# Performance work log

Hardware: AMD Instinct MI355X
Metric: run time of the kernel (lower is better)

## Reference

```python
import jax, jax.numpy as jnp
import numpy as np

EMBED_DIM = 256
NUM_HEADS = 8
PROJ_DIM = EMBED_DIM // NUM_HEADS


def setup_inputs() -> dict:
    key = jax.random.key(0)
    ks = jax.random.split(key, 5)
    scale = 1.0 / np.sqrt(EMBED_DIM)
    inputs = jax.random.normal(ks[0], (2, 12, 12, 12, EMBED_DIM), dtype=jnp.float32)
    Wq = jax.random.normal(ks[1], (EMBED_DIM, EMBED_DIM), dtype=jnp.float32) * scale
    Wk = jax.random.normal(ks[2], (EMBED_DIM, EMBED_DIM), dtype=jnp.float32) * scale
    Wv = jax.random.normal(ks[3], (EMBED_DIM, EMBED_DIM), dtype=jnp.float32) * scale
    Wo = jax.random.normal(ks[4], (EMBED_DIM, EMBED_DIM), dtype=jnp.float32) * scale
    z = jnp.zeros((EMBED_DIM,), dtype=jnp.float32)
    return {"inputs": inputs, "Wq": Wq, "bq": z, "Wk": Wk, "bk": z,
            "Wv": Wv, "bv": z, "Wo": Wo, "bo": z}


def reference(inputs, Wq, bq, Wk, bk, Wv, bv, Wo, bo):
    B, h, w, d, E = inputs.shape
    S = h * w * d  # flattened spatial sequence
    x = inputs.reshape(B, S, E)
    # projections + head split: [B, S, E] -> [B, H, S, P]
    def split_heads(t):
        return t.reshape(B, S, NUM_HEADS, PROJ_DIM).transpose(0, 2, 1, 3)
    q = split_heads(x @ Wq + bq)
    k = split_heads(x @ Wk + bk)
    v = split_heads(x @ Wv + bv)
    # NOTE: original module does NOT scale by 1/sqrt(proj_dim)
    scores = jnp.einsum('bhsp,bhtp->bhst', q, k)  # [B, H, S, S]
    attn = jax.nn.softmax(scores, axis=-1)
    out = jnp.einsum('bhst,bhtp->bhsp', attn, v)  # [B, H, S, P]
    out = out.transpose(0, 2, 1, 3).reshape(B, h, w, d, E)
    return out @ Wo + bo
```

## Files before the change

kernel.cpp:

```cpp
#include <hip/hip_runtime.h>
#include <math.h>

#define EMBED 256
#define HEADS 8
#define PDIM  32
#define BATCH 2
#define SEQ   1728
#define NTOK  (BATCH*SEQ)
#define NE    (NTOK*EMBED)
#define NKT   (SEQ/64)
#define LOG2E 1.44269504088896f

typedef __attribute__((ext_vector_type(8))) __bf16 bf16x8;
typedef __attribute__((ext_vector_type(4))) float  f32x4;
typedef unsigned short ushort_t;
typedef unsigned int   uint_t;

static __device__ __forceinline__ unsigned short f2bf_rne(float f) {
    union { float f; unsigned u; } x; x.f = f;
    unsigned r = x.u + 0x7fffu + ((x.u >> 16) & 1u);
    return (unsigned short)(r >> 16);
}
union v8cast { uint4 u; bf16x8 v; };

static __device__ __forceinline__ void cvt8_hilo(const float f[8], bf16x8& hi, bf16x8& lo) {
    uint4 ph, pl;
    uint_t* phv = (uint_t*)&ph; uint_t* plv = (uint_t*)&pl;
    #pragma unroll
    for (int j = 0; j < 4; ++j) {
        const float f0 = f[2 * j], f1 = f[2 * j + 1];
        const uint_t u0 = __float_as_uint(f0) + 0x8000u;
        const uint_t u1 = __float_as_uint(f1) + 0x8000u;
        phv[j] = __builtin_amdgcn_perm(u1, u0, 0x07060302u);
        const float l0 = f0 - __uint_as_float(u0 & 0xFFFF0000u);
        const float l1 = f1 - __uint_as_float(u1 & 0xFFFF0000u);
        plv[j] = __builtin_amdgcn_perm(__float_as_uint(l1) + 0x8000u,
                                       __float_as_uint(l0) + 0x8000u, 0x07060302u);
    }
    v8cast ch; ch.u = ph; hi = ch.v;
    v8cast cl; cl.u = pl; lo = cl.v;
}

__global__ __launch_bounds__(64) void qkv_gemm_kernel(
    const float* __restrict__ x,
    const float* __restrict__ Wq, const float* __restrict__ bq,
    const float* __restrict__ Wk, const float* __restrict__ bk,
    const float* __restrict__ Wv, const float* __restrict__ bv,
    ushort_t* __restrict__ qo, ushort_t* __restrict__ ko, ushort_t* __restrict__ vt)
{
    const int lane = threadIdx.x, li = lane & 15, quad = lane >> 4;
    const int m0 = blockIdx.x * 64, n0 = blockIdx.y * 32, z = blockIdx.z;
    const float* __restrict__ W    = (z == 0) ? Wq : (z == 1) ? Wk : Wv;
    const float* __restrict__ bias = (z == 0) ? bq : (z == 1) ? bk : bv;

    const float* ap = x + (size_t)(m0 + li) * EMBED + quad * 8;

    f32x4 acc[4][2];
    #pragma unroll
    for (int mt = 0; mt < 4; ++mt)
        #pragma unroll
        for (int nt = 0; nt < 2; ++nt)
            acc[mt][nt] = (f32x4){0.f, 0.f, 0.f, 0.f};

    #pragma unroll 2
    for (int k0 = 0; k0 < EMBED; k0 += 32) {
        bf16x8 ah[4], al[4];
        #pragma unroll
        for (int mt = 0; mt < 4; ++mt) {
            float af[8];
            *(float4*)&af[0] = *(const float4*)(ap + (size_t)mt * 16 * EMBED + k0);
            *(float4*)&af[4] = *(const float4*)(ap + (size_t)mt * 16 * EMBED + k0 + 4);
            cvt8_hilo(af, ah[mt], al[mt]);
        }
        bf16x8 bh[2], bl[2];
        #pragma unroll
        for (int nt = 0; nt < 2; ++nt) {
            const int n = n0 + nt * 16 + li;
            const float* wp = W + (size_t)(k0 + quad * 8) * EMBED + n;
            float bf[8];
            #pragma unroll
            for (int jj = 0; jj < 8; ++jj) bf[jj] = wp[(size_t)jj * EMBED];
            cvt8_hilo(bf, bh[nt], bl[nt]);
        }
        #pragma unroll
        for (int mt = 0; mt < 4; ++mt)
            #pragma unroll
            for (int nt = 0; nt < 2; ++nt) {
                acc[mt][nt] = __builtin_amdgcn_mfma_f32_16x16x32_bf16(ah[mt], bh[nt], acc[mt][nt], 0, 0, 0);
                acc[mt][nt] = __builtin_amdgcn_mfma_f32_16x16x32_bf16(al[mt], bh[nt], acc[mt][nt], 0, 0, 0);
                acc[mt][nt] = __builtin_amdgcn_mfma_f32_16x16x32_bf16(ah[mt], bl[nt], acc[mt][nt], 0, 0, 0);
            }
    }

    const int b = m0 / SEQ;
    const int sbase = m0 - b * SEQ;

    if (z <= 1) {
        ushort_t* __restrict__ dst = z ? ko : qo;
        #pragma unroll
        for (int nt = 0; nt < 2; ++nt) {
            const int gcol = n0 + nt * 16 + li;
            const int h = gcol >> 5, p = gcol & 31;
            const float bb = bias[gcol];
            ushort_t* base = dst + ((size_t)(b * HEADS + h) * SEQ) * PDIM + p;
            #pragma unroll
            for (int mt = 0; mt < 4; ++mt)
                #pragma unroll
                for (int r = 0; r < 4; ++r) {
                    const int s = sbase + mt * 16 + quad * 4 + r;
                    base[(size_t)s * PDIM] = f2bf_rne(acc[mt][nt][r] + bb);
                }
        }
    } else {
        #pragma unroll
        for (int nt = 0; nt < 2; ++nt) {
            const int gcol = n0 + nt * 16 + li;
            const int h = gcol >> 5, p = gcol & 31;
            const float bb = bias[gcol];
            ushort_t* base = vt + ((size_t)(b * HEADS + h) * PDIM + p) * SEQ;
            #pragma unroll
            for (int mt = 0; mt < 4; ++mt) {
                const int s0 = sbase + mt * 16 + quad * 4;
                ushort4 w;
                w.x = f2bf_rne(acc[mt][nt][0] + bb);
                w.y = f2bf_rne(acc[mt][nt][1] + bb);
                w.z = f2bf_rne(acc[mt][nt][2] + bb);
                w.w = f2bf_rne(acc[mt][nt][3] + bb);
                *(ushort4*)&base[s0] = w;
            }
        }
    }
}

__global__ __launch_bounds__(256) void attn_kernel(
    const ushort_t* __restrict__ q, const ushort_t* __restrict__ k,
    const ushort_t* __restrict__ vt, ushort_t* __restrict__ aob)
{
    const int t    = threadIdx.x;
    const int lane = t & 63;
    const int w    = t >> 6;
    const int li   = lane & 15;
    const int quad = lane >> 4;
    const int bh = blockIdx.y;
    const int b  = bh >> 3, h = bh & 7;
    const int q0 = blockIdx.x * 64 + w * 16;

    const ushort_t* __restrict__ qb = q  + (size_t)bh * SEQ * PDIM;
    const ushort_t* __restrict__ kb = k  + (size_t)bh * SEQ * PDIM;
    const ushort_t* __restrict__ vb = vt + (size_t)bh * PDIM * SEQ;

    __shared__ ushort_t Ks[2][64][40];
    __shared__ ushort_t Vs[2][32][72];
    __shared__ ushort_t Ps[4][16][72];

    const bf16x8 qfrag = *(const bf16x8*)(qb + (size_t)(q0 + li) * PDIM + quad * 8);

    const int jk = w * 16 + (lane >> 2), ck = (lane & 3) * 8;
    const int pv = w * 8 + (lane >> 3),  cv = (lane & 7) * 8;
    const ushort_t* kgp = kb + (size_t)jk * PDIM + ck;
    const ushort_t* vgp = vb + (size_t)pv * SEQ + cv;

    f32x4 o0 = {0.f, 0.f, 0.f, 0.f};
    f32x4 o1 = {0.f, 0.f, 0.f, 0.f};
    float m_run = -__builtin_inff(), l_run = 0.f;

    uint4 kreg = *(const uint4*)(kgp);
    uint4 vreg = *(const uint4*)(vgp);

    for (int kt = 0; kt < NKT; ++kt) {
        const int p = kt & 1;
        *(uint4*)&Ks[p][jk][ck] = kreg;
        *(uint4*)&Vs[p][pv][cv] = vreg;
        __syncthreads();
        if (kt + 1 < NKT) {
            kreg = *(const uint4*)(kgp + (size_t)(kt + 1) * 64 * PDIM);
            vreg = *(const uint4*)(vgp + (kt + 1) * 64);
        }

        const f32x4 zero = {0.f, 0.f, 0.f, 0.f};
        f32x4 st[4];
        #pragma unroll
        for (int jt = 0; jt < 4; ++jt) {
            const bf16x8 kf = *(const bf16x8*)&Ks[p][jt * 16 + li][quad * 8];
            st[jt] = __builtin_amdgcn_mfma_f32_16x16x32_bf16(kf, qfrag, zero, 0, 0, 0);
        }

        float tm = st[0][0];
        #pragma unroll
        for (int jt = 0; jt < 4; ++jt)
            #pragma unroll
            for (int r = 0; r < 4; ++r) tm = fmaxf(tm, st[jt][r]);
        tm = fmaxf(tm, __shfl_xor(tm, 16));
        tm = fmaxf(tm, __shfl_xor(tm, 32));
        const float mnew  = fmaxf(m_run, tm);
        const float negml = -(mnew * LOG2E);

        float ps = 0.f;
        #pragma unroll
        for (int jt = 0; jt < 4; ++jt) {
            const float p0 = __builtin_amdgcn_exp2f(fmaf(st[jt][0], LOG2E, negml));
            const float p1 = __builtin_amdgcn_exp2f(fmaf(st[jt][1], LOG2E, negml));
            const float p2 = __builtin_amdgcn_exp2f(fmaf(st[jt][2], LOG2E, negml));
            const float p3 = __builtin_amdgcn_exp2f(fmaf(st[jt][3], LOG2E, negml));
            ps += (p0 + p1) + (p2 + p3);
            uint2 pw;
            pw.x = __builtin_amdgcn_perm(__float_as_uint(p1) + 0x8000u,
                                         __float_as_uint(p0) + 0x8000u, 0x07060302u);
            pw.y = __builtin_amdgcn_perm(__float_as_uint(p3) + 0x8000u,
                                         __float_as_uint(p2) + 0x8000u, 0x07060302u);
            *(uint2*)&Ps[w][li][16 * jt + 4 * quad] = pw;
        }
        ps += __shfl_xor(ps, 16);
        ps += __shfl_xor(ps, 32);

        const float alpha = __builtin_amdgcn_exp2f(fmaf(m_run, LOG2E, negml));
        l_run = fmaf(l_run, alpha, ps);
        m_run = mnew;

        float af[4];
        #pragma unroll
        for (int r = 0; r < 4; ++r) af[r] = __shfl(alpha, 4 * quad + r);
        #pragma unroll
        for (int r = 0; r < 4; ++r) { o0[r] *= af[r]; o1[r] *= af[r]; }

        const bf16x8 pa0 = *(const bf16x8*)&Ps[w][li][8 * quad];
        const bf16x8 pa1 = *(const bf16x8*)&Ps[w][li][32 + 8 * quad];
        const bf16x8 vf00 = *(const bf16x8*)&Vs[p][li][quad * 8];
        const bf16x8 vf01 = *(const bf16x8*)&Vs[p][16 + li][quad * 8];
        const bf16x8 vf10 = *(const bf16x8*)&Vs[p][li][32 + quad * 8];
        const bf16x8 vf11 = *(const bf16x8*)&Vs[p][16 + li][32 + quad * 8];
        o0 = __builtin_amdgcn_mfma_f32_16x16x32_bf16(pa0, vf00, o0, 0, 0, 0);
        o0 = __builtin_amdgcn_mfma_f32_16x16x32_bf16(pa1, vf10, o0, 0, 0, 0);
        o1 = __builtin_amdgcn_mfma_f32_16x16x32_bf16(pa0, vf01, o1, 0, 0, 0);
        o1 = __builtin_amdgcn_mfma_f32_16x16x32_bf16(pa1, vf11, o1, 0, 0, 0);
    }

    float linv[4];
    #pragma unroll
    for (int r = 0; r < 4; ++r) linv[r] = 1.0f / __shfl(l_run, 4 * quad + r);
    #pragma unroll
    for (int r = 0; r < 4; ++r) {
        const int s = q0 + 4 * quad + r;
        ushort_t* row = aob + ((size_t)(b * SEQ + s)) * EMBED + h * PDIM;
        row[li]      = f2bf_rne(o0[r] * linv[r]);
        row[16 + li] = f2bf_rne(o1[r] * linv[r]);
    }
}

__global__ __launch_bounds__(64) void out_gemm_kernel(
    const ushort_t* __restrict__ a, const float* __restrict__ Wo,
    const float* __restrict__ bo, float* __restrict__ out)
{
    const int lane = threadIdx.x, li = lane & 15, quad = lane >> 4;
    const int m0 = blockIdx.x * 64, n0 = blockIdx.y * 16;

    const ushort_t* aph = a + (size_t)(m0 + li) * EMBED + quad * 8;

    f32x4 acc[4];
    #pragma unroll
    for (int mt = 0; mt < 4; ++mt) acc[mt] = (f32x4){0.f, 0.f, 0.f, 0.f};

    #pragma unroll 2
    for (int k0 = 0; k0 < EMBED; k0 += 32) {
        bf16x8 ah[4];
        #pragma unroll
        for (int mt = 0; mt < 4; ++mt)
            ah[mt] = *(const bf16x8*)(aph + (size_t)mt * 16 * EMBED + k0);
        const float* wp = Wo + (size_t)(k0 + quad * 8) * EMBED + n0 + li;
        uint4 pb;
        uint_t* pbv = (uint_t*)&pb;
        #pragma unroll
        for (int j = 0; j < 4; ++j) {
            const uint_t u0 = __float_as_uint(wp[(size_t)(2 * j) * EMBED])     + 0x8000u;
            const uint_t u1 = __float_as_uint(wp[(size_t)(2 * j + 1) * EMBED]) + 0x8000u;
            pbv[j] = __builtin_amdgcn_perm(u1, u0, 0x07060302u);
        }
        v8cast cb; cb.u = pb;
        #pragma unroll
        for (int mt = 0; mt < 4; ++mt)
            acc[mt] = __builtin_amdgcn_mfma_f32_16x16x32_bf16(ah[mt], cb.v, acc[mt], 0, 0, 0);
    }

    const float bb = bo[n0 + li];
    #pragma unroll
    for (int mt = 0; mt < 4; ++mt)
        #pragma unroll
        for (int r = 0; r < 4; ++r) {
            const int row = m0 + mt * 16 + quad * 4 + r;
            out[(size_t)row * EMBED + n0 + li] = acc[mt][r] + bb;
        }
}

extern "C" void kernel_launch(void* const* d_in, const int* in_sizes, int n_in,
                              void* d_out, int out_size, void* d_ws, size_t ws_size,
                              hipStream_t stream)
{
    const float* x  = (const float*)d_in[0];
    const float* Wq = (const float*)d_in[1];
    const float* bq = (const float*)d_in[2];
    const float* Wk = (const float*)d_in[3];
    const float* bk = (const float*)d_in[4];
    const float* Wv = (const float*)d_in[5];
    const float* bv = (const float*)d_in[6];
    const float* Wo = (const float*)d_in[7];
    const float* bo = (const float*)d_in[8];
    float* out = (float*)d_out;

    ushort_t* ws  = (ushort_t*)d_ws;
    ushort_t* qb  = ws;
    ushort_t* kb  = qb + (size_t)NE;
    ushort_t* vt  = kb + (size_t)NE;
    ushort_t* aob = vt + (size_t)NE;

    qkv_gemm_kernel<<<dim3(NTOK / 64, 8, 3), 64, 0, stream>>>(
        x, Wq, bq, Wk, bk, Wv, bv, qb, kb, vt);
    attn_kernel<<<dim3(SEQ / 64, BATCH * HEADS), 256, 0, stream>>>(qb, kb, vt, aob);
    out_gemm_kernel<<<dim3(NTOK / 64, 16), 64, 0, stream>>>(aob, Wo, bo, out);
}
```

Measured before the change: 119.9 us.

## Add prep kernel for bf16 split/transposed weights and split attention KV across waves

A new prep kernel converts x and the Q/K/V weights into hi/lo bf16 pairs once, and stores the weights transposed. It also converts Wo to transposed bf16. The QKV and output GEMMs then load bf16 directly instead of doing strided fp32 loads and converting inside each tile, and their M tiles are halved to launch more blocks. The attention kernel doubles to 512 threads, with two waves per query group each processing alternate key tiles, and merges the partial softmax states through shared memory at the end. This adds an extra kernel launch, workspace traffic and a shared-memory reduction in exchange for more parallelism and less redundant conversion.

```diff
diff --git a/kernel.cpp b/kernel.cpp
--- a/kernel.cpp
+++ b/kernel.cpp
@@ -9,6 +9,10 @@
 #define NTOK  (BATCH*SEQ)
 #define NE    (NTOK*EMBED)
 #define NKT   (SEQ/64)
+#define NPAIR ((NKT+1)/2)
+#define WSZ   (EMBED*EMBED)
+#define XCH   (NE/8)
+#define WCH   (WSZ/8)
 #define LOG2E 1.44269504088896f
 
 typedef __attribute__((ext_vector_type(8))) __bf16 bf16x8;
@@ -41,49 +45,81 @@
     v8cast cl; cl.u = pl; lo = cl.v;
 }
 
+__global__ __launch_bounds__(256) void prep_kernel(
+    const float* __restrict__ x,
+    const float* __restrict__ Wq, const float* __restrict__ Wk,
+    const float* __restrict__ Wv, const float* __restrict__ Wo,
+    ushort_t* __restrict__ xhi, ushort_t* __restrict__ xlo,
+    ushort_t* __restrict__ wthi, ushort_t* __restrict__ wtlo,
+    ushort_t* __restrict__ wot)
+{
+    const int id = blockIdx.x * 256 + threadIdx.x;
+    if (id < XCH) {
+        float f[8];
+        *(float4*)&f[0] = *(const float4*)(x + (size_t)id * 8);
+        *(float4*)&f[4] = *(const float4*)(x + (size_t)id * 8 + 4);
+        bf16x8 hi, lo; cvt8_hilo(f, hi, lo);
+        v8cast ch; ch.v = hi; *(uint4*)&xhi[(size_t)id * 8] = ch.u;
+        v8cast cl; cl.v = lo; *(uint4*)&xlo[(size_t)id * 8] = cl.u;
+    } else if (id < XCH + 3 * WCH) {
+        int r = id - XCH;
+        const int z = r / WCH; r -= z * WCH;
+        const float* __restrict__ W = (z == 0) ? Wq : (z == 1) ? Wk : Wv;
+        const int n = r >> 5, kc = (r & 31) * 8;
+        float f[8];
+        #pragma unroll
+        for (int j = 0; j < 8; ++j) f[j] = W[(size_t)(kc + j) * EMBED + n];
+        bf16x8 hi, lo; cvt8_hilo(f, hi, lo);
+        v8cast ch; ch.v = hi; *(uint4*)&wthi[(size_t)z * WSZ + n * EMBED + kc] = ch.u;
+        v8cast cl; cl.v = lo; *(uint4*)&wtlo[(size_t)z * WSZ + n * EMBED + kc] = cl.u;
+    } else {
+        int r = id - XCH - 3 * WCH;
+        const int n = r >> 5, kc = (r & 31) * 8;
+        float f[8];
+        #pragma unroll
+        for (int j = 0; j < 8; ++j) f[j] = Wo[(size_t)(kc + j) * EMBED + n];
+        bf16x8 hi, lo; cvt8_hilo(f, hi, lo);
+        v8cast ch; ch.v = hi; *(uint4*)&wot[n * EMBED + kc] = ch.u;
+    }
+}
+
 __global__ __launch_bounds__(64) void qkv_gemm_kernel(
-    const float* __restrict__ x,
-    const float* __restrict__ Wq, const float* __restrict__ bq,
-    const float* __restrict__ Wk, const float* __restrict__ bk,
-    const float* __restrict__ Wv, const float* __restrict__ bv,
+    const ushort_t* __restrict__ xhi, const ushort_t* __restrict__ xlo,
+    const ushort_t* __restrict__ wthi, const ushort_t* __restrict__ wtlo,
+    const float* __restrict__ bq, const float* __restrict__ bk, const float* __restrict__ bv,
     ushort_t* __restrict__ qo, ushort_t* __restrict__ ko, ushort_t* __restrict__ vt)
 {
     const int lane = threadIdx.x, li = lane & 15, quad = lane >> 4;
-    const int m0 = blockIdx.x * 64, n0 = blockIdx.y * 32, z = blockIdx.z;
-    const float* __restrict__ W    = (z == 0) ? Wq : (z == 1) ? Wk : Wv;
+    const int m0 = blockIdx.x * 32, n0 = blockIdx.y * 32, z = blockIdx.z;
     const float* __restrict__ bias = (z == 0) ? bq : (z == 1) ? bk : bv;
 
-    const float* ap = x + (size_t)(m0 + li) * EMBED + quad * 8;
-
-    f32x4 acc[4][2];
-    #pragma unroll
-    for (int mt = 0; mt < 4; ++mt)
+    const ushort_t* ahp = xhi + (size_t)(m0 + li) * EMBED + quad * 8;
+    const ushort_t* alp = xlo + (size_t)(m0 + li) * EMBED + quad * 8;
+    const ushort_t* bhp = wthi + (size_t)z * WSZ + (size_t)(n0 + li) * EMBED + quad * 8;
+    const ushort_t* blp = wtlo + (size_t)z * WSZ + (size_t)(n0 + li) * EMBED + quad * 8;
+
+    f32x4 acc[2][2];
+    #pragma unroll
+    for (int mt = 0; mt < 2; ++mt)
         #pragma unroll
         for (int nt = 0; nt < 2; ++nt)
             acc[mt][nt] = (f32x4){0.f, 0.f, 0.f, 0.f};
 
     #pragma unroll 2
     for (int k0 = 0; k0 < EMBED; k0 += 32) {
-        bf16x8 ah[4], al[4];
-        #pragma unroll
-        for (int mt = 0; mt < 4; ++mt) {
-            float af[8];
-            *(float4*)&af[0] = *(const float4*)(ap + (size_t)mt * 16 * EMBED + k0);
-            *(float4*)&af[4] = *(const float4*)(ap + (size_t)mt * 16 * EMBED + k0 + 4);
-            cvt8_hilo(af, ah[mt], al[mt]);
-        }
-        bf16x8 bh[2], bl[2];
+        bf16x8 ah[2], al[2], bh[2], bl[2];
+        #pragma unroll
+        for (int mt = 0; mt < 2; ++mt) {
+            ah[mt] = *(const bf16x8*)(ahp + (size_t)mt * 16 * EMBED + k0);
+            al[mt] = *(const bf16x8*)(alp + (size_t)mt * 16 * EMBED + k0);
+        }
         #pragma unroll
         for (int nt = 0; nt < 2; ++nt) {
-            const int n = n0 + nt * 16 + li;
-            const float* wp = W + (size_t)(k0 + quad * 8) * EMBED + n;
-            float bf[8];
-            #pragma unroll
-            for (int jj = 0; jj < 8; ++jj) bf[jj] = wp[(size_t)jj * EMBED];
-            cvt8_hilo(bf, bh[nt], bl[nt]);
-        }
-        #pragma unroll
-        for (int mt = 0; mt < 4; ++mt)
+            bh[nt] = *(const bf16x8*)(bhp + (size_t)nt * 16 * EMBED + k0);
+            bl[nt] = *(const bf16x8*)(blp + (size_t)nt * 16 * EMBED + k0);
+        }
+        #pragma unroll
+        for (int mt = 0; mt < 2; ++mt)
             #pragma unroll
             for (int nt = 0; nt < 2; ++nt) {
                 acc[mt][nt] = __builtin_amdgcn_mfma_f32_16x16x32_bf16(ah[mt], bh[nt], acc[mt][nt], 0, 0, 0);
@@ -104,7 +140,7 @@
             const float bb = bias[gcol];
             ushort_t* base = dst + ((size_t)(b * HEADS + h) * SEQ) * PDIM + p;
             #pragma unroll
-            for (int mt = 0; mt < 4; ++mt)
+            for (int mt = 0; mt < 2; ++mt)
                 #pragma unroll
                 for (int r = 0; r < 4; ++r) {
                     const int s = sbase + mt * 16 + quad * 4 + r;
@@ -119,7 +155,7 @@
             const float bb = bias[gcol];
             ushort_t* base = vt + ((size_t)(b * HEADS + h) * PDIM + p) * SEQ;
             #pragma unroll
-            for (int mt = 0; mt < 4; ++mt) {
+            for (int mt = 0; mt < 2; ++mt) {
                 const int s0 = sbase + mt * 16 + quad * 4;
                 ushort4 w;
                 w.x = f2bf_rne(acc[mt][nt][0] + bb);
@@ -132,7 +168,7 @@
     }
 }
 
-__global__ __launch_bounds__(256) void attn_kernel(
+__global__ __launch_bounds__(512, 4) void attn_kernel(
     const ushort_t* __restrict__ q, const ushort_t* __restrict__ k,
     const ushort_t* __restrict__ vt, ushort_t* __restrict__ aob)
 {
@@ -141,24 +177,28 @@
     const int w    = t >> 6;
     const int li   = lane & 15;
     const int quad = lane >> 4;
+    const int qg   = w >> 1, half = w & 1;
     const int bh = blockIdx.y;
     const int b  = bh >> 3, h = bh & 7;
-    const int q0 = blockIdx.x * 64 + w * 16;
+    const int q0 = blockIdx.x * 64 + qg * 16;
 
     const ushort_t* __restrict__ qb = q  + (size_t)bh * SEQ * PDIM;
     const ushort_t* __restrict__ kb = k  + (size_t)bh * SEQ * PDIM;
     const ushort_t* __restrict__ vb = vt + (size_t)bh * PDIM * SEQ;
 
-    __shared__ ushort_t Ks[2][64][40];
-    __shared__ ushort_t Vs[2][32][72];
-    __shared__ ushort_t Ps[4][16][72];
+    __shared__ ushort_t Ks[2][2][64][40];
+    __shared__ ushort_t Vs[2][2][32][72];
+    __shared__ ushort_t Ps[8][16][72];
+    __shared__ float    Om[8][16][33];
+    __shared__ float    Ml[8][2][16];
 
     const bf16x8 qfrag = *(const bf16x8*)(qb + (size_t)(q0 + li) * PDIM + quad * 8);
 
-    const int jk = w * 16 + (lane >> 2), ck = (lane & 3) * 8;
-    const int pv = w * 8 + (lane >> 3),  cv = (lane & 7) * 8;
-    const ushort_t* kgp = kb + (size_t)jk * PDIM + ck;
-    const ushort_t* vgp = vb + (size_t)pv * SEQ + cv;
+    const int ktil = t >> 8;
+    const int krow = (t >> 2) & 63, kck = (t & 3) * 8;
+    const int vrow = (t >> 3) & 31, vcv = (t & 7) * 8;
+    const ushort_t* kgp = kb + (size_t)(ktil * 64 + krow) * PDIM + kck;
+    const ushort_t* vgp = vb + (size_t)vrow * SEQ + ktil * 64 + vcv;
 
     f32x4 o0 = {0.f, 0.f, 0.f, 0.f};
     f32x4 o1 = {0.f, 0.f, 0.f, 0.f};
@@ -167,123 +207,133 @@
     uint4 kreg = *(const uint4*)(kgp);
     uint4 vreg = *(const uint4*)(vgp);
 
-    for (int kt = 0; kt < NKT; ++kt) {
-        const int p = kt & 1;
-        *(uint4*)&Ks[p][jk][ck] = kreg;
-        *(uint4*)&Vs[p][pv][cv] = vreg;
+    #pragma unroll 2
+    for (int i = 0; i < NPAIR; ++i) {
+        const int p = i & 1;
+        *(uint4*)&Ks[p][ktil][krow][kck] = kreg;
+        *(uint4*)&Vs[p][ktil][vrow][vcv] = vreg;
         __syncthreads();
-        if (kt + 1 < NKT) {
-            kreg = *(const uint4*)(kgp + (size_t)(kt + 1) * 64 * PDIM);
-            vreg = *(const uint4*)(vgp + (kt + 1) * 64);
-        }
-
-        const f32x4 zero = {0.f, 0.f, 0.f, 0.f};
-        f32x4 st[4];
-        #pragma unroll
-        for (int jt = 0; jt < 4; ++jt) {
-            const bf16x8 kf = *(const bf16x8*)&Ks[p][jt * 16 + li][quad * 8];
-            st[jt] = __builtin_amdgcn_mfma_f32_16x16x32_bf16(kf, qfrag, zero, 0, 0, 0);
-        }
-
-        float tm = st[0][0];
-        #pragma unroll
-        for (int jt = 0; jt < 4; ++jt)
-            #pragma unroll
-            for (int r = 0; r < 4; ++r) tm = fmaxf(tm, st[jt][r]);
-        tm = fmaxf(tm, __shfl_xor(tm, 16));
-        tm = fmaxf(tm, __shfl_xor(tm, 32));
-        const float mnew  = fmaxf(m_run, tm);
-        const float negml = -(mnew * LOG2E);
-
-        float ps = 0.f;
-        #pragma unroll
-        for (int jt = 0; jt < 4; ++jt) {
-            const float p0 = __builtin_amdgcn_exp2f(fmaf(st[jt][0], LOG2E, negml));
-            const float p1 = __builtin_amdgcn_exp2f(fmaf(st[jt][1], LOG2E, negml));
-            const float p2 = __builtin_amdgcn_exp2f(fmaf(st[jt][2], LOG2E, negml));
-            const float p3 = __builtin_amdgcn_exp2f(fmaf(st[jt][3], LOG2E, negml));
-            ps += (p0 + p1) + (p2 + p3);
-            uint2 pw;
-            pw.x = __builtin_amdgcn_perm(__float_as_uint(p1) + 0x8000u,
-                                         __float_as_uint(p0) + 0x8000u, 0x07060302u);
-            pw.y = __builtin_amdgcn_perm(__float_as_uint(p3) + 0x8000u,
-                                         __float_as_uint(p2) + 0x8000u, 0x07060302u);
-            *(uint2*)&Ps[w][li][16 * jt + 4 * quad] = pw;
-        }
-        ps += __shfl_xor(ps, 16);
-        ps += __shfl_xor(ps, 32);
-
-        const float alpha = __builtin_amdgcn_exp2f(fmaf(m_run, LOG2E, negml));
-        l_run = fmaf(l_run, alpha, ps);
-        m_run = mnew;
-
-        float af[4];
-        #pragma unroll
-        for (int r = 0; r < 4; ++r) af[r] = __shfl(alpha, 4 * quad + r);
-        #pragma unroll
-        for (int r = 0; r < 4; ++r) { o0[r] *= af[r]; o1[r] *= af[r]; }
-
-        const bf16x8 pa0 = *(const bf16x8*)&Ps[w][li][8 * quad];
-        const bf16x8 pa1 = *(const bf16x8*)&Ps[w][li][32 + 8 * quad];
-        const bf16x8 vf00 = *(const bf16x8*)&Vs[p][li][quad * 8];
-        const bf16x8 vf01 = *(const bf16x8*)&Vs[p][16 + li][quad * 8];
-        const bf16x8 vf10 = *(const bf16x8*)&Vs[p][li][32 + quad * 8];
-        const bf16x8 vf11 = *(const bf16x8*)&Vs[p][16 + li][32 + quad * 8];
-        o0 = __builtin_amdgcn_mfma_f32_16x16x32_bf16(pa0, vf00, o0, 0, 0, 0);
-        o0 = __builtin_amdgcn_mfma_f32_16x16x32_bf16(pa1, vf10, o0, 0, 0, 0);
-        o1 = __builtin_amdgcn_mfma_f32_16x16x32_bf16(pa0, vf01, o1, 0, 0, 0);
-        o1 = __builtin_amdgcn_mfma_f32_16x16x32_bf16(pa1, vf11, o1, 0, 0, 0);
-    }
-
-    float linv[4];
-    #pragma unroll
-    for (int r = 0; r < 4; ++r) linv[r] = 1.0f / __shfl(l_run, 4 * quad + r);
+        if (i + 1 < NPAIR && 2 * (i + 1) + ktil < NKT) {
+            kreg = *(const uint4*)(kgp + (size_t)(2 * (i + 1)) * 64 * PDIM);
+            vreg = *(const uint4*)(vgp + 2 * (i + 1) * 64);
+        }
+        const int kt = 2 * i + half;
+        if (kt < NKT) {
+            const f32x4 zero = {0.f, 0.f, 0.f, 0.f};
+            f32x4 st[4];
+            #pragma unroll
+            for (int jt = 0; jt < 4; ++jt) {
+                const bf16x8 kf = *(const bf16x8*)&Ks[p][half][jt * 16 + li][quad * 8];
+                st[jt] = __builtin_amdgcn_mfma_f32_16x16x32_bf16(kf, qfrag, zero, 0, 0, 0);
+            }
+
+            float tm = fmaxf(fmaxf(fmaxf(st[0][0], st[0][1]), fmaxf(st[0][2], st[0][3])),
+                             fmaxf(fmaxf(st[1][0], st[1][1]), fmaxf(st[1][2], st[1][3])));
+            tm = fmaxf(tm, fmaxf(fmaxf(fmaxf(st[2][0], st[2][1]), fmaxf(st[2][2], st[2][3])),
+                                 fmaxf(fmaxf(st[3][0], st[3][1]), fmaxf(st[3][2], st[3][3]))));
+            tm = fmaxf(tm, __shfl_xor(tm, 16));
+            tm = fmaxf(tm, __shfl_xor(tm, 32));
+            const float mnew  = fmaxf(m_run, tm);
+            const float negml = -(mnew * LOG2E);
+
+            float ps = 0.f;
+            #pragma unroll
+            for (int jt = 0; jt < 4; ++jt) {
+                const float p0 = __builtin_amdgcn_exp2f(fmaf(st[jt][0], LOG2E, negml));
+                const float p1 = __builtin_amdgcn_exp2f(fmaf(st[jt][1], LOG2E, negml));
+                const float p2 = __builtin_amdgcn_exp2f(fmaf(st[jt][2], LOG2E, negml));
+                const float p3 = __builtin_amdgcn_exp2f(fmaf(st[jt][3], LOG2E, negml));
+                ps += (p0 + p1) + (p2 + p3);
+                uint2 pw;
+                pw.x = __builtin_amdgcn_perm(__float_as_uint(p1) + 0x8000u,
+                                             __float_as_uint(p0) + 0x8000u, 0x07060302u);
+                pw.y = __builtin_amdgcn_perm(__float_as_uint(p3) + 0x8000u,
+                                             __float_as_uint(p2) + 0x8000u, 0x07060302u);
+                *(uint2*)&Ps[w][li][16 * jt + 4 * quad] = pw;
+            }
+            ps += __shfl_xor(ps, 16);
+            ps += __shfl_xor(ps, 32);
+
+            const float alpha = __builtin_amdgcn_exp2f(fmaf(m_run, LOG2E, negml));
+            l_run = fmaf(l_run, alpha, ps);
+            m_run = mnew;
+
+            float af[4];
+            #pragma unroll
+            for (int r = 0; r < 4; ++r) af[r] = __shfl(alpha, 4 * quad + r);
+            #pragma unroll
+            for (int r = 0; r < 4; ++r) { o0[r] *= af[r]; o1[r] *= af[r]; }
+
+            const bf16x8 pa0 = *(const bf16x8*)&Ps[w][li][8 * quad];
+            const bf16x8 pa1 = *(const bf16x8*)&Ps[w][li][32 + 8 * quad];
+            const bf16x8 vf00 = *(const bf16x8*)&Vs[p][half][li][quad * 8];
+            const bf16x8 vf01 = *(const bf16x8*)&Vs[p][half][16 + li][quad * 8];
+            const bf16x8 vf10 = *(const bf16x8*)&Vs[p][half][li][32 + quad * 8];
+            const bf16x8 vf11 = *(const bf16x8*)&Vs[p][half][16 + li][32 + quad * 8];
+            o0 = __builtin_amdgcn_mfma_f32_16x16x32_bf16(pa0, vf00, o0, 0, 0, 0);
+            o0 = __builtin_amdgcn_mfma_f32_16x16x32_bf16(pa1, vf10, o0, 0, 0, 0);
+            o1 = __builtin_amdgcn_mfma_f32_16x16x32_bf16(pa0, vf01, o1, 0, 0, 0);
+            o1 = __builtin_amdgcn_mfma_f32_16x16x32_bf16(pa1, vf11, o1, 0, 0, 0);
+        }
+    }
+
     #pragma unroll
     for (int r = 0; r < 4; ++r) {
-        const int s = q0 + 4 * quad + r;
-        ushort_t* row = aob + ((size_t)(b * SEQ + s)) * EMBED + h * PDIM;
-        row[li]      = f2bf_rne(o0[r] * linv[r]);
-        row[16 + li] = f2bf_rne(o1[r] * linv[r]);
+        Om[w][4 * quad + r][li]      = o0[r];
+        Om[w][4 * quad + r][16 + li] = o1[r];
+    }
+    if (quad == 0) { Ml[w][0][li] = m_run; Ml[w][1][li] = l_run; }
+    __syncthreads();
+
+    const int wa = qg * 2, wb = wa + 1;
+    const float ma = Ml[wa][0][li], mb = Ml[wb][0][li];
+    const float mC = fmaxf(ma, mb);
+    const float sa = __builtin_amdgcn_exp2f((ma - mC) * LOG2E);
+    const float sb = __builtin_amdgcn_exp2f((mb - mC) * LOG2E);
+    const float lC = Ml[wa][1][li] * sa + Ml[wb][1][li] * sb;
+    const float inv = 1.0f / lC;
+    const float fa = sa * inv, fb = sb * inv;
+    const int c = half * 16 + li;
+    #pragma unroll
+    for (int r = 0; r < 4; ++r) {
+        const int qq = 4 * quad + r;
+        const float aq = __shfl(fa, qq);
+        const float bq_ = __shfl(fb, qq);
+        const float val = Om[wa][qq][c] * aq + Om[wb][qq][c] * bq_;
+        const int s = q0 + qq;
+        aob[((size_t)(b * SEQ + s)) * EMBED + h * PDIM + c] = f2bf_rne(val);
     }
 }
 
 __global__ __launch_bounds__(64) void out_gemm_kernel(
-    const ushort_t* __restrict__ a, const float* __restrict__ Wo,
+    const ushort_t* __restrict__ a, const ushort_t* __restrict__ wot,
     const float* __restrict__ bo, float* __restrict__ out)
 {
     const int lane = threadIdx.x, li = lane & 15, quad = lane >> 4;
-    const int m0 = blockIdx.x * 64, n0 = blockIdx.y * 16;
-
-    const ushort_t* aph = a + (size_t)(m0 + li) * EMBED + quad * 8;
-
-    f32x4 acc[4];
-    #pragma unroll
-    for (int mt = 0; mt < 4; ++mt) acc[mt] = (f32x4){0.f, 0.f, 0.f, 0.f};
+    const int m0 = blockIdx.x * 32, n0 = blockIdx.y * 16;
+
+    const ushort_t* ap = a + (size_t)(m0 + li) * EMBED + quad * 8;
+    const ushort_t* bp = wot + (size_t)(n0 + li) * EMBED + quad * 8;
+
+    f32x4 acc[2];
+    #pragma unroll
+    for (int mt = 0; mt < 2; ++mt) acc[mt] = (f32x4){0.f, 0.f, 0.f, 0.f};
 
     #pragma unroll 2
     for (int k0 = 0; k0 < EMBED; k0 += 32) {
-        bf16x8 ah[4];
-        #pragma unroll
-        for (int mt = 0; mt < 4; ++mt)
-            ah[mt] = *(const bf16x8*)(aph + (size_t)mt * 16 * EMBED + k0);
-        const float* wp = Wo + (size_t)(k0 + quad * 8) * EMBED + n0 + li;
-        uint4 pb;
-        uint_t* pbv = (uint_t*)&pb;
-        #pragma unroll
-        for (int j = 0; j < 4; ++j) {
-            const uint_t u0 = __float_as_uint(wp[(size_t)(2 * j) * EMBED])     + 0x8000u;
-            const uint_t u1 = __float_as_uint(wp[(size_t)(2 * j + 1) * EMBED]) + 0x8000u;
-            pbv[j] = __builtin_amdgcn_perm(u1, u0, 0x07060302u);
-        }
-        v8cast cb; cb.u = pb;
-        #pragma unroll
-        for (int mt = 0; mt < 4; ++mt)
-            acc[mt] = __builtin_amdgcn_mfma_f32_16x16x32_bf16(ah[mt], cb.v, acc[mt], 0, 0, 0);
+        bf16x8 ah[2];
+        #pragma unroll
+        for (int mt = 0; mt < 2; ++mt)
+            ah[mt] = *(const bf16x8*)(ap + (size_t)mt * 16 * EMBED + k0);
+        const bf16x8 bf = *(const bf16x8*)(bp + k0);
+        #pragma unroll
+        for (int mt = 0; mt < 2; ++mt)
+            acc[mt] = __builtin_amdgcn_mfma_f32_16x16x32_bf16(ah[mt], bf, acc[mt], 0, 0, 0);
     }
 
     const float bb = bo[n0 + li];
     #pragma unroll
-    for (int mt = 0; mt < 4; ++mt)
+    for (int mt = 0; mt < 2; ++mt)
         #pragma unroll
         for (int r = 0; r < 4; ++r) {
             const int row = m0 + mt * 16 + quad * 4 + r;
@@ -306,14 +356,21 @@
     const float* bo = (const float*)d_in[8];
     float* out = (float*)d_out;
 
-    ushort_t* ws  = (ushort_t*)d_ws;
-    ushort_t* qb  = ws;
-    ushort_t* kb  = qb + (size_t)NE;
-    ushort_t* vt  = kb + (size_t)NE;
-    ushort_t* aob = vt + (size_t)NE;
-
-    qkv_gemm_kernel<<<dim3(NTOK / 64, 8, 3), 64, 0, stream>>>(
-        x, Wq, bq, Wk, bk, Wv, bv, qb, kb, vt);
-    attn_kernel<<<dim3(SEQ / 64, BATCH * HEADS), 256, 0, stream>>>(qb, kb, vt, aob);
-    out_gemm_kernel<<<dim3(NTOK / 64, 16), 64, 0, stream>>>(aob, Wo, bo, out);
-}
+    ushort_t* ws   = (ushort_t*)d_ws;
+    ushort_t* qb   = ws;
+    ushort_t* kb   = qb   + (size_t)NE;
+    ushort_t* vtb  = kb   + (size_t)NE;
+    ushort_t* aob  = vtb  + (size_t)NE;
+    ushort_t* xhi  = aob  + (size_t)NE;
+    ushort_t* xlo  = xhi  + (size_t)NE;
+    ushort_t* wthi = xlo  + (size_t)NE;
+    ushort_t* wtlo = wthi + (size_t)(3 * WSZ);
+    ushort_t* wot  = wtlo + (size_t)(3 * WSZ);
+
+    prep_kernel<<<dim3((XCH + 4 * WCH) / 256), 256, 0, stream>>>(
+        x, Wq, Wk, Wv, Wo, xhi, xlo, wthi, wtlo, wot);
+    qkv_gemm_kernel<<<dim3(NTOK / 32, 8, 3), 64, 0, stream>>>(
+        xhi, xlo, wthi, wtlo, bq, bk, bv, qb, kb, vtb);
+    attn_kernel<<<dim3(SEQ / 64, BATCH * HEADS), 512, 0, stream>>>(qb, kb, vtb, aob);
+    out_gemm_kernel<<<dim3(NTOK / 32, 16), 64, 0, stream>>>(aob, wot, bo, out);
+}
```

Result: slower. 127.7 us (+6.5%).
